# Optimization experiments

Hardware: AMD Instinct MI355X
Metric: run time of the kernel (lower is better)

Reference implementation:

```python
import jax, jax.numpy as jnp
import numpy as np

L, B, H, NI, V = 256, 32, 1024, 1024, 10000


def setup_inputs() -> dict:
    key = jax.random.key(0)
    ks = jax.random.split(key, 8)
    return {
        "input_ids": jax.random.randint(ks[0], (L, B), 0, V),
        "h0": jnp.zeros((B, H), jnp.float32),
        "c0": jnp.zeros((B, H), jnp.float32),
        "emb_w": jax.random.uniform(ks[1], (V, NI), jnp.float32, -0.1, 0.1),
        "w_ih": jax.random.normal(ks[2], (4 * H, NI), jnp.float32) * 0.02,
        "w_hh": jax.random.normal(ks[3], (4 * H, H), jnp.float32) * 0.02,
        "dec_w": jax.random.uniform(ks[4], (V, H), jnp.float32, -0.1, 0.1),
        "dec_b": jnp.zeros((V,), jnp.float32),
        "W": jax.random.normal(ks[5], (H, 1), jnp.float32) * 0.1,
        "U": jax.random.normal(ks[6], (H, 1), jnp.float32) * 0.1,
    }


def reference(input_ids, h0, c0, emb_w, w_ih, w_hh, dec_w, dec_b, W, U):
    seq_len, bsz = input_ids.shape
    nhid = h0.shape[1]
    emb = emb_w[input_ids]  # [L, B, NI]

    def lstm_cell(x, h, c):
        # torch LSTMCell (bias=False), gate order i, f, g, o
        gates = x @ w_ih.T + h @ w_hh.T  # [B, 4H]
        i, f, g, o = jnp.split(gates, 4, axis=-1)
        c_new = jax.nn.sigmoid(f) * c + jax.nn.sigmoid(i) * jnp.tanh(g)
        h_new = jax.nn.sigmoid(o) * jnp.tanh(c_new)
        return h_new, c_new

    time_idx = jnp.arange(seq_len)

    def step(carry, xs):
        h, c, hist = carry  # hist: [L, B, H] padded history of hiddens
        x, i = xs
        h, c = lstm_cell(x, h, c)
        hist = hist.at[i].set(h)
        # additive attention over all hiddens so far
        b = (hist.reshape(-1, nhid) @ U).reshape(seq_len, bsz)  # [L, B]
        a = (h @ W).reshape(1, bsz)  # [1, B]
        scores = jnp.tanh(a + b)
        scores = jnp.where((time_idx <= i)[:, None], scores, -jnp.inf)
        att = jax.nn.softmax(scores, axis=0)  # softmax over time
        ctx = jnp.sum(att[:, :, None] * hist, axis=0)  # [B, H]
        return (h, c, hist), ctx

    hist0 = jnp.zeros((seq_len, bsz, nhid), dtype=h0.dtype)
    (h, c, _), ctx = jax.lax.scan(step, (h0, c0, hist0), (emb, time_idx))
    # ctx: [L, B, H]
    logits = ctx @ dec_w.T + dec_b  # [L, B, V]
    out = jax.nn.log_softmax(logits, axis=-1)
    return out, (h, c)
```

## Files before the change

kernel.cpp:

```cpp
#include <hip/hip_runtime.h>
#include <math.h>

typedef unsigned short u16;
typedef unsigned u32;
typedef float f32x4 __attribute__((ext_vector_type(4)));
typedef float f32x2 __attribute__((ext_vector_type(2)));
typedef __bf16 bf16x8 __attribute__((ext_vector_type(8)));
typedef u16 u16x8 __attribute__((ext_vector_type(8)));
typedef u16 u16x4 __attribute__((ext_vector_type(4)));
typedef u32 u32x4 __attribute__((ext_vector_type(4)));

#define L_SEQ 256
#define BSZ 32
#define HID 1024
#define NIN 1024
#define VOC 10000
#define G4 4096
#define MROWS 8192
#define NB 64
#define DPB 16
#define SENT 0xFFFFFFFFu

__device__ __forceinline__ u16 f2bf(float f) {
    unsigned u = __float_as_uint(f);
    unsigned r = u + 0x7FFFu + ((u >> 16) & 1u);
    return (u16)(r >> 16);
}
#define BF2F(x) __builtin_bit_cast(float, (u32)((u16)(x)) << 16)

__device__ __forceinline__ float fast_sigm(float x) {
    x = fminf(fmaxf(x, -15.f), 15.f);
    return __builtin_amdgcn_rcpf(1.f + __expf(-x));
}
__device__ __forceinline__ float fast_tanh(float x) {
    x = fminf(fmaxf(x, -15.f), 15.f);
    float t = __expf(2.f * x);
    return (t - 1.f) * __builtin_amdgcn_rcpf(t + 1.f);
}
__device__ __forceinline__ unsigned umax4(u16x8 v) {
    u32x4 c = __builtin_bit_cast(u32x4, v);
    unsigned a = c.x > c.y ? c.x : c.y;
    unsigned b = c.z > c.w ? c.z : c.w;
    return a > b ? a : b;
}

__global__ __launch_bounds__(256) void cvt_bf16_kernel(const float* __restrict__ in,
                                                       u16* __restrict__ out, int n4) {
    int idx = blockIdx.x * 256 + threadIdx.x;
    if (idx < n4) {
        f32x4 v = *(const f32x4*)(in + (size_t)idx * 4);
        u16x4 o = {f2bf(v.x), f2bf(v.y), f2bf(v.z), f2bf(v.w)};
        *(u16x4*)(out + (size_t)idx * 4) = o;
    }
}

__global__ __launch_bounds__(256) void gather_emb_kernel(const int* __restrict__ ids,
                                                         const float* __restrict__ emb_w,
                                                         u16* __restrict__ out) {
    int m = blockIdx.x;
    int id = ids[m];
    const float* src = emb_w + (size_t)id * NIN;
    u16* dst = out + (size_t)m * NIN;
    int t = threadIdx.x;
    f32x4 v = *(const f32x4*)(src + t * 4);
    u16x4 o = {f2bf(v.x), f2bf(v.y), f2bf(v.z), f2bf(v.w)};
    *(u16x4*)(dst + t * 4) = o;
}

__global__ __launch_bounds__(256) void gemm_gxT_kernel(const u16* __restrict__ A,
                                                       const u16* __restrict__ B,
                                                       float* __restrict__ gxT) {
    int m0 = blockIdx.x * 128;
    int n0 = blockIdx.y * 128;
    __shared__ alignas(16) u16 As[128][40];
    __shared__ alignas(16) u16 Bs[128][40];
    int t = threadIdx.x;
    int lane = t & 63, wave = t >> 6;
    int wr = wave >> 1, wc = wave & 1;
    int l15 = lane & 15, l4 = lane >> 4;

    f32x4 acc[4][4];
    f32x4 zv = {0.f, 0.f, 0.f, 0.f};
    for (int mi = 0; mi < 4; ++mi)
        for (int ni = 0; ni < 4; ++ni) acc[mi][ni] = zv;

    for (int k0 = 0; k0 < NIN; k0 += 32) {
        for (int s = 0; s < 2; ++s) {
            int task = t + s * 256;
            int row = task >> 2, kof = (task & 3) * 8;
            *(u16x8*)(&As[row][kof]) = *(const u16x8*)(A + (size_t)(m0 + row) * NIN + k0 + kof);
            *(u16x8*)(&Bs[row][kof]) = *(const u16x8*)(B + (size_t)(n0 + row) * NIN + k0 + kof);
        }
        __syncthreads();
        bf16x8 af[4], bfr[4];
        for (int mi = 0; mi < 4; ++mi)
            af[mi] = __builtin_bit_cast(bf16x8, *(const u16x8*)(&As[wr * 64 + mi * 16 + l15][l4 * 8]));
        for (int ni = 0; ni < 4; ++ni)
            bfr[ni] = __builtin_bit_cast(bf16x8, *(const u16x8*)(&Bs[wc * 64 + ni * 16 + l15][l4 * 8]));
        for (int mi = 0; mi < 4; ++mi)
            for (int ni = 0; ni < 4; ++ni)
                acc[mi][ni] = __builtin_amdgcn_mfma_f32_16x16x32_bf16(af[mi], bfr[ni], acc[mi][ni], 0, 0, 0);
        __syncthreads();
    }
    for (int mi = 0; mi < 4; ++mi)
        for (int ni = 0; ni < 4; ++ni) {
            int n = n0 + wc * 64 + ni * 16 + l15;
            int g = n >> 10, dd = n & 1023;
            int dblk = dd >> 4, dl = dd & 15;
            int mbase = m0 + wr * 64 + mi * 16 + l4 * 4;
            int i = mbase >> 5, bb = mbase & 31;
            size_t idx = ((((size_t)dblk * L_SEQ + i) * 4 + g) * 16 + dl) * 32 + bb;
            *(f32x4*)(&gxT[idx]) = acc[mi][ni];
        }
}

__global__ __launch_bounds__(256) void gemm_bt_kernel(const u16* __restrict__ A,
                                                      const u16* __restrict__ B,
                                                      float* __restrict__ C,
                                                      const float* __restrict__ bias,
                                                      int M, int N, int K) {
    int m0 = blockIdx.x * 128;
    int n0 = blockIdx.y * 128;
    __shared__ alignas(16) u16 As[128][40];
    __shared__ alignas(16) u16 Bs[128][40];
    int t = threadIdx.x;
    int lane = t & 63, wave = t >> 6;
    int wr = wave >> 1, wc = wave & 1;
    int l15 = lane & 15, l4 = lane >> 4;

    f32x4 acc[4][4];
    f32x4 zv = {0.f, 0.f, 0.f, 0.f};
    for (int mi = 0; mi < 4; ++mi)
        for (int ni = 0; ni < 4; ++ni) acc[mi][ni] = zv;

    for (int k0 = 0; k0 < K; k0 += 32) {
        for (int s = 0; s < 2; ++s) {
            int task = t + s * 256;
            int row = task >> 2, kof = (task & 3) * 8;
            u16x8 av = *(const u16x8*)(A + (size_t)(m0 + row) * K + k0 + kof);
            *(u16x8*)(&As[row][kof]) = av;
            int brow = n0 + row;
            u16x8 bv = {0, 0, 0, 0, 0, 0, 0, 0};
            if (brow < N) bv = *(const u16x8*)(B + (size_t)brow * K + k0 + kof);
            *(u16x8*)(&Bs[row][kof]) = bv;
        }
        __syncthreads();
        bf16x8 af[4], bfr[4];
        for (int mi = 0; mi < 4; ++mi)
            af[mi] = __builtin_bit_cast(bf16x8, *(const u16x8*)(&As[wr * 64 + mi * 16 + l15][l4 * 8]));
        for (int ni = 0; ni < 4; ++ni)
            bfr[ni] = __builtin_bit_cast(bf16x8, *(const u16x8*)(&Bs[wc * 64 + ni * 16 + l15][l4 * 8]));
        for (int mi = 0; mi < 4; ++mi)
            for (int ni = 0; ni < 4; ++ni)
                acc[mi][ni] = __builtin_amdgcn_mfma_f32_16x16x32_bf16(af[mi], bfr[ni], acc[mi][ni], 0, 0, 0);
        __syncthreads();
    }

    for (int mi = 0; mi < 4; ++mi)
        for (int ni = 0; ni < 4; ++ni) {
            int col = n0 + wc * 64 + ni * 16 + l15;
            if (col < N) {
                float bb = bias ? bias[col] : 0.f;
                int rbase = m0 + wr * 64 + mi * 16 + l4 * 4;
                for (int r = 0; r < 4; ++r)
                    C[(size_t)(rbase + r) * N + col] = acc[mi][ni][r] + bb;
            }
        }
}

__global__ __launch_bounds__(256, 1) void lstm_seq_kernel(
    const float* __restrict__ c0, const u16* __restrict__ w_hh_bf,
    const float* __restrict__ gxT, const float* __restrict__ Wv, const float* __restrict__ Uv,
    u16* __restrict__ hb_hist, float* __restrict__ out_tail, float* __restrict__ part_ab) {
    __shared__ alignas(16) u16 Bs[64][1024];
    __shared__ float gsm[4][32][17];
    __shared__ float c_sl[32][17];

    int blk = blockIdx.x;
    int d0 = blk * DPB;
    int t = threadIdx.x;
    int lane = t & 63, wave = t >> 6;
    int wm = wave & 1, wn = wave >> 1;
    int l15 = lane & 15, l4 = lane >> 4;

    for (int s = 0; s < 32; ++s) {
        int cid = t + s * 256;
        int c = cid >> 7;
        int ch = cid & 127;
        int g = c >> 4, dl = c & 15;
        u16x8 v = *(const u16x8*)(w_hh_bf + (size_t)(g * HID + d0 + dl) * HID + ch * 8);
        int chs = ch ^ (c & 7);
        *(u16x8*)(&Bs[c][chs * 8]) = v;
    }
    for (int s = t; s < 512; s += 256) {
        int b = s >> 4, dl = s & 15;
        c_sl[b][dl] = c0[b * HID + d0 + dl];
    }
    __syncthreads();

    int cA = wn * 32 + l15;
    int cB = cA + 16;
    int sw = cA & 7;
    int gA = cA >> 4, dA = cA & 15;
    int gB = cB >> 4, dB = cB & 15;

    int bb = t >> 3;
    int pr = t & 7;
    int dl0 = pr * 2;

    const float* gxTb = gxT + (size_t)blk * ((size_t)L_SEQ * 2048) + wm * 16 + l4 * 4;

    f32x4 gxa0 = *(const f32x4*)(gxTb + (size_t)0 * 2048 + gA * 512 + dA * 32);
    f32x4 gxa1 = *(const f32x4*)(gxTb + (size_t)0 * 2048 + gB * 512 + dB * 32);

    for (int i = 0; i < L_SEQ; ++i) {
        const u16* hb = hb_hist + (size_t)i * (BSZ * HID);
        const u16* aptr = hb + (size_t)(wm * 16 + l15) * HID + l4 * 8;

        u16x8 afr[32];
#pragma unroll
        for (int kk = 0; kk < 32; ++kk)
            asm volatile("global_load_dwordx4 %0, %1, off offset:%c2 sc0 sc1"
                         : "=v"(afr[kk])
                         : "v"(aptr), "n"(kk * 64));

        f32x4 acc0 = {0.f, 0.f, 0.f, 0.f}, acc1 = {0.f, 0.f, 0.f, 0.f};
        unsigned pend = 0xFFFFFFFFu;
        for (;;) {
            asm volatile("s_waitcnt vmcnt(0)" ::: "memory");
            __builtin_amdgcn_sched_barrier(0);
            unsigned done = 0;
#pragma unroll
            for (int kk = 0; kk < 32; ++kk) {
                if (pend & (1u << kk)) {
                    if (__ballot(umax4(afr[kk]) == SENT) == 0) {
                        bf16x8 af = __builtin_bit_cast(bf16x8, afr[kk]);
                        int ch = kk * 4 + l4;
                        bf16x8 b0 = __builtin_bit_cast(bf16x8, *(const u16x8*)(&Bs[cA][(ch ^ sw) * 8]));
                        bf16x8 b1 = __builtin_bit_cast(bf16x8, *(const u16x8*)(&Bs[cB][(ch ^ sw) * 8]));
                        acc0 = __builtin_amdgcn_mfma_f32_16x16x32_bf16(af, b0, acc0, 0, 0, 0);
                        acc1 = __builtin_amdgcn_mfma_f32_16x16x32_bf16(af, b1, acc1, 0, 0, 0);
                        done |= 1u << kk;
                    }
                }
            }
            pend &= ~done;
            if (!pend) break;
#pragma unroll
            for (int kk = 0; kk < 32; ++kk)
                if (pend & (1u << kk))
                    asm volatile("global_load_dwordx4 %0, %1, off offset:%c2 sc0 sc1"
                                 : "=v"(afr[kk])
                                 : "v"(aptr), "n"(kk * 64));
            __builtin_amdgcn_s_sleep(1);
        }
        __builtin_amdgcn_sched_barrier(0);

#pragma unroll
        for (int r = 0; r < 4; ++r) {
            int m = wm * 16 + l4 * 4 + r;
            gsm[gA][m][dA] = acc0[r] + gxa0[r];
            gsm[gB][m][dB] = acc1[r] + gxa1[r];
        }
        __syncthreads();

        u16* hb_next = hb_hist + (size_t)(i + 1) * (BSZ * HID);
        float hn01[2];
#pragma unroll
        for (int q = 0; q < 2; ++q) {
            int dl = dl0 + q;
            float ig = gsm[0][bb][dl], fg = gsm[1][bb][dl];
            float gg = gsm[2][bb][dl], og = gsm[3][bb][dl];
            float cn = fast_sigm(fg) * c_sl[bb][dl] + fast_sigm(ig) * fast_tanh(gg);
            float hn = fast_sigm(og) * fast_tanh(cn);
            c_sl[bb][dl] = cn;
            hn01[q] = hn;
        }
        unsigned pk = (unsigned)f2bf(hn01[0]) | ((unsigned)f2bf(hn01[1]) << 16);
        __hip_atomic_store((unsigned*)(hb_next + bb * HID + d0 + dl0), pk,
                           __ATOMIC_RELAXED, __HIP_MEMORY_SCOPE_AGENT);
        if (i == L_SEQ - 1) {
            f32x2 hv = {hn01[0], hn01[1]};
            *(f32x2*)(out_tail + (size_t)bb * HID + d0 + dl0) = hv;
        }
        float pa = hn01[0] * Wv[d0 + dl0] + hn01[1] * Wv[d0 + dl0 + 1];
        float pb = hn01[0] * Uv[d0 + dl0] + hn01[1] * Uv[d0 + dl0 + 1];
        pa += __shfl_xor(pa, 1); pb += __shfl_xor(pb, 1);
        pa += __shfl_xor(pa, 2); pb += __shfl_xor(pb, 2);
        pa += __shfl_xor(pa, 4); pb += __shfl_xor(pb, 4);
        if (pr == 0) {
            f32x2 pv = {pa, pb};
            *(f32x2*)(part_ab + (((size_t)i * NB + blk) * BSZ + bb) * 2) = pv;
        }

        int inx = (i + 1 < L_SEQ) ? i + 1 : i;
        gxa0 = *(const f32x4*)(gxTb + (size_t)inx * 2048 + gA * 512 + dA * 32);
        gxa1 = *(const f32x4*)(gxTb + (size_t)inx * 2048 + gB * 512 + dB * 32);
    }

    for (int s = t; s < 512; s += 256) {
        int b2 = s >> 4, dl = s & 15;
        out_tail[(size_t)BSZ * HID + b2 * HID + d0 + dl] = c_sl[b2][dl];
    }
}

__global__ __launch_bounds__(256) void reduce_ab_kernel(const float* __restrict__ part_ab,
                                                        float* __restrict__ a_arr,
                                                        float* __restrict__ b_arr) {
    int i = blockIdx.x;
    int t = threadIdx.x;
    int b = t & 31, q = t >> 5;
    float sa = 0.f, sb = 0.f;
    for (int j = 0; j < 8; ++j) {
        int blk = q * 8 + j;
        f32x2 v = *(const f32x2*)(part_ab + (((size_t)i * NB + blk) * BSZ + b) * 2);
        sa += v.x;
        sb += v.y;
    }
    __shared__ float ra[8][32], rb[8][32];
    ra[q][b] = sa;
    rb[q][b] = sb;
    __syncthreads();
    if (q == 0) {
        for (int j = 1; j < 8; ++j) { sa += ra[j][b]; sb += rb[j][b]; }
        a_arr[i * BSZ + b] = sa;
        b_arr[i * BSZ + b] = sb;
    }
}

__global__ __launch_bounds__(256) void attn_kernel(const float* __restrict__ a_arr,
                                                   const float* __restrict__ b_arr,
                                                   const u16* __restrict__ hb_hist,
                                                   u16* __restrict__ ctx_bf) {
    int b = blockIdx.y;
    int i0 = blockIdx.x * 8;
    int t = threadIdx.x;
    __shared__ float att[8][256];
    __shared__ float red[256];

    float bt = b_arr[t * BSZ + b];
    for (int q = 0; q < 8; ++q) {
        int iq = i0 + q;
        att[q][t] = (t <= iq) ? tanhf(a_arr[iq * BSZ + b] + bt) : -INFINITY;
    }
    __syncthreads();
    for (int q = 0; q < 8; ++q) {
        int iq = i0 + q;
        red[t] = att[q][t];
        __syncthreads();
        for (int s = 128; s > 0; s >>= 1) {
            if (t < s) red[t] = fmaxf(red[t], red[t + s]);
            __syncthreads();
        }
        float m = red[0];
        __syncthreads();
        float e = (t <= iq) ? expf(att[q][t] - m) : 0.f;
        red[t] = e;
        __syncthreads();
        for (int s = 128; s > 0; s >>= 1) {
            if (t < s) red[t] += red[t + s];
            __syncthreads();
        }
        float sum = red[0];
        __syncthreads();
        att[q][t] = e / sum;
        __syncthreads();
    }

    int hc = t * 4;
    f32x4 accq[8];
    f32x4 zv = {0.f, 0.f, 0.f, 0.f};
    for (int q = 0; q < 8; ++q) accq[q] = zv;
    int imax = i0 + 7;
    for (int t2 = 0; t2 <= imax; ++t2) {
        u16x4 hq = *(const u16x4*)(hb_hist + (size_t)(t2 + 1) * (BSZ * HID) + (size_t)b * HID + hc);
        f32x4 hv = {BF2F(hq.x), BF2F(hq.y), BF2F(hq.z), BF2F(hq.w)};
        for (int q = 0; q < 8; ++q) accq[q] += hv * att[q][t2];
    }
    for (int q = 0; q < 8; ++q) {
        size_t row = (size_t)(i0 + q) * BSZ + b;
        u16x4 o = {f2bf(accq[q].x), f2bf(accq[q].y), f2bf(accq[q].z), f2bf(accq[q].w)};
        *(u16x4*)(ctx_bf + row * HID + hc) = o;
    }
}

__global__ __launch_bounds__(256) void logsoftmax_kernel(float* __restrict__ x, int V) {
    int row = blockIdx.x;
    float* p = x + (size_t)row * V;
    __shared__ float red[256];
    int t = threadIdx.x;
    float frag[40];
    float m = -INFINITY;
#pragma unroll
    for (int k = 0; k < 40; ++k) {
        int j = t + k * 256;
        if (j < VOC) {
            frag[k] = p[j];
            m = fmaxf(m, frag[k]);
        }
    }
    red[t] = m;
    __syncthreads();
    for (int s = 128; s > 0; s >>= 1) {
        if (t < s) red[t] = fmaxf(red[t], red[t + s]);
        __syncthreads();
    }
    m = red[0];
    __syncthreads();
    float sum = 0.f;
#pragma unroll
    for (int k = 0; k < 40; ++k) {
        int j = t + k * 256;
        if (j < VOC) sum += __expf(frag[k] - m);
    }
    red[t] = sum;
    __syncthreads();
    for (int s = 128; s > 0; s >>= 1) {
        if (t < s) red[t] += red[t + s];
        __syncthreads();
    }
    float lse = m + logf(red[0]);
#pragma unroll
    for (int k = 0; k < 40; ++k) {
        int j = t + k * 256;
        if (j < VOC) p[j] = frag[k] - lse;
    }
}

extern "C" void kernel_launch(void* const* d_in, const int* in_sizes, int n_in,
                              void* d_out, int out_size, void* d_ws, size_t ws_size,
                              hipStream_t stream) {
    const int* ids = (const int*)d_in[0];
    const float* h0 = (const float*)d_in[1];
    const float* c0 = (const float*)d_in[2];
    const float* emb_w = (const float*)d_in[3];
    const float* w_ih = (const float*)d_in[4];
    const float* w_hh = (const float*)d_in[5];
    const float* dec_w = (const float*)d_in[6];
    const float* dec_b = (const float*)d_in[7];
    const float* Wv = (const float*)d_in[8];
    const float* Uv = (const float*)d_in[9];

    char* p = (char*)d_ws;
    auto alloc = [&](size_t bytes) {
        void* r = (void*)p;
        p += (bytes + 255) & ~(size_t)255;
        return r;
    };
    u16* w_ih_bf = (u16*)alloc((size_t)G4 * NIN * 2);
    u16* w_hh_bf = (u16*)alloc((size_t)G4 * HID * 2);
    u16* dec_w_bf = (u16*)alloc((size_t)VOC * HID * 2);
    char* hbreg = (char*)alloc((size_t)(L_SEQ + 1) * BSZ * HID * 2);
    u16* ctx_bf = (u16*)alloc((size_t)MROWS * HID * 2);
    float* part_ab = (float*)alloc((size_t)L_SEQ * NB * BSZ * 2 * 4);
    float* a_arr = (float*)alloc((size_t)L_SEQ * BSZ * 4);
    float* b_arr = (float*)alloc((size_t)L_SEQ * BSZ * 4);

    u16* A_emb = (u16*)hbreg;
    u16* hb_hist = (u16*)hbreg;
    float* out = (float*)d_out;
    float* gxT = out;
    float* out_tail = out + (size_t)MROWS * VOC;

    cvt_bf16_kernel<<<G4 * NIN / 1024, 256, 0, stream>>>(w_ih, w_ih_bf, G4 * NIN / 4);
    cvt_bf16_kernel<<<G4 * HID / 1024, 256, 0, stream>>>(w_hh, w_hh_bf, G4 * HID / 4);
    cvt_bf16_kernel<<<(VOC * HID / 4 + 255) / 256, 256, 0, stream>>>(dec_w, dec_w_bf, VOC * HID / 4);
    gather_emb_kernel<<<MROWS, 256, 0, stream>>>(ids, emb_w, A_emb);
    gemm_gxT_kernel<<<dim3(MROWS / 128, G4 / 128), 256, 0, stream>>>(A_emb, w_ih_bf, gxT);

    hipMemsetAsync(hb_hist + (size_t)BSZ * HID, 0xFF, (size_t)L_SEQ * BSZ * HID * 2, stream);
    cvt_bf16_kernel<<<BSZ * HID / 1024, 256, 0, stream>>>(h0, hb_hist, BSZ * HID / 4);

    {
        const float* c0a = c0;
        const u16* whha = w_hh_bf;
        const float* gxa = gxT;
        const float* Wa = Wv;
        const float* Ua = Uv;
        u16* hba = hb_hist;
        float* tail = out_tail;
        float* pab = part_ab;
        void* args[] = {&c0a, &whha, &gxa, &Wa, &Ua, &hba, &tail, &pab};
        hipLaunchCooperativeKernel((const void*)lstm_seq_kernel, dim3(NB), dim3(256), args, 0,
                                   stream);
    }
    reduce_ab_kernel<<<L_SEQ, 256, 0, stream>>>(part_ab, a_arr, b_arr);
    attn_kernel<<<dim3(L_SEQ / 8, BSZ), 256, 0, stream>>>(a_arr, b_arr, hb_hist, ctx_bf);
    gemm_bt_kernel<<<dim3(MROWS / 128, (VOC + 127) / 128), 256, 0, stream>>>(ctx_bf, dec_w_bf, out,
                                                                             dec_b, MROWS, VOC, HID);
    logsoftmax_kernel<<<MROWS, 256, 0, stream>>>(out, VOC);
}
```

Before: 2.605 ms.

## Overlap input-projection GEMM with LSTM recurrence via producer blocks and sentinel polling

Removes the separate input-projection GEMM launch and runs it inside the recurrent kernel on 160 extra worker blocks, which write the gate pre-activations as bf16 with atomic stores. The 64 recurrent blocks poll a sentinel-filled buffer before consuming each timestep's values, so the GEMM can overlap the serial recurrence. The projection output is also stored in bf16 instead of fp32, halving its traffic, at some cost in precision. The kernel is now a normal launch rather than a cooperative one, so correctness depends on the producer blocks being co-resident with the recurrent blocks and making progress; otherwise it could deadlock.

```diff
diff --git a/kernel.cpp b/kernel.cpp
--- a/kernel.cpp
+++ b/kernel.cpp
@@ -3,12 +3,14 @@
 
 typedef unsigned short u16;
 typedef unsigned u32;
+typedef unsigned long long u64;
 typedef float f32x4 __attribute__((ext_vector_type(4)));
 typedef float f32x2 __attribute__((ext_vector_type(2)));
 typedef __bf16 bf16x8 __attribute__((ext_vector_type(8)));
 typedef u16 u16x8 __attribute__((ext_vector_type(8)));
 typedef u16 u16x4 __attribute__((ext_vector_type(4)));
 typedef u32 u32x4 __attribute__((ext_vector_type(4)));
+typedef u32 u32x2 __attribute__((ext_vector_type(2)));
 
 #define L_SEQ 256
 #define BSZ 32
@@ -18,6 +20,7 @@
 #define G4 4096
 #define MROWS 8192
 #define NB 64
+#define NW 160
 #define DPB 16
 #define SENT 0xFFFFFFFFu
 
@@ -65,53 +68,6 @@
     f32x4 v = *(const f32x4*)(src + t * 4);
     u16x4 o = {f2bf(v.x), f2bf(v.y), f2bf(v.z), f2bf(v.w)};
     *(u16x4*)(dst + t * 4) = o;
-}
-
-__global__ __launch_bounds__(256) void gemm_gxT_kernel(const u16* __restrict__ A,
-                                                       const u16* __restrict__ B,
-                                                       float* __restrict__ gxT) {
-    int m0 = blockIdx.x * 128;
-    int n0 = blockIdx.y * 128;
-    __shared__ alignas(16) u16 As[128][40];
-    __shared__ alignas(16) u16 Bs[128][40];
-    int t = threadIdx.x;
-    int lane = t & 63, wave = t >> 6;
-    int wr = wave >> 1, wc = wave & 1;
-    int l15 = lane & 15, l4 = lane >> 4;
-
-    f32x4 acc[4][4];
-    f32x4 zv = {0.f, 0.f, 0.f, 0.f};
-    for (int mi = 0; mi < 4; ++mi)
-        for (int ni = 0; ni < 4; ++ni) acc[mi][ni] = zv;
-
-    for (int k0 = 0; k0 < NIN; k0 += 32) {
-        for (int s = 0; s < 2; ++s) {
-            int task = t + s * 256;
-            int row = task >> 2, kof = (task & 3) * 8;
-            *(u16x8*)(&As[row][kof]) = *(const u16x8*)(A + (size_t)(m0 + row) * NIN + k0 + kof);
-            *(u16x8*)(&Bs[row][kof]) = *(const u16x8*)(B + (size_t)(n0 + row) * NIN + k0 + kof);
-        }
-        __syncthreads();
-        bf16x8 af[4], bfr[4];
-        for (int mi = 0; mi < 4; ++mi)
-            af[mi] = __builtin_bit_cast(bf16x8, *(const u16x8*)(&As[wr * 64 + mi * 16 + l15][l4 * 8]));
-        for (int ni = 0; ni < 4; ++ni)
-            bfr[ni] = __builtin_bit_cast(bf16x8, *(const u16x8*)(&Bs[wc * 64 + ni * 16 + l15][l4 * 8]));
-        for (int mi = 0; mi < 4; ++mi)
-            for (int ni = 0; ni < 4; ++ni)
-                acc[mi][ni] = __builtin_amdgcn_mfma_f32_16x16x32_bf16(af[mi], bfr[ni], acc[mi][ni], 0, 0, 0);
-        __syncthreads();
-    }
-    for (int mi = 0; mi < 4; ++mi)
-        for (int ni = 0; ni < 4; ++ni) {
-            int n = n0 + wc * 64 + ni * 16 + l15;
-            int g = n >> 10, dd = n & 1023;
-            int dblk = dd >> 4, dl = dd & 15;
-            int mbase = m0 + wr * 64 + mi * 16 + l4 * 4;
-            int i = mbase >> 5, bb = mbase & 31;
-            size_t idx = ((((size_t)dblk * L_SEQ + i) * 4 + g) * 16 + dl) * 32 + bb;
-            *(f32x4*)(&gxT[idx]) = acc[mi][ni];
-        }
 }
 
 __global__ __launch_bounds__(256) void gemm_bt_kernel(const u16* __restrict__ A,
@@ -169,19 +125,73 @@
 }
 
 __global__ __launch_bounds__(256, 1) void lstm_seq_kernel(
-    const float* __restrict__ c0, const u16* __restrict__ w_hh_bf,
-    const float* __restrict__ gxT, const float* __restrict__ Wv, const float* __restrict__ Uv,
-    u16* __restrict__ hb_hist, float* __restrict__ out_tail, float* __restrict__ part_ab) {
+    const float* __restrict__ c0, const u16* __restrict__ w_hh_bf, u16* __restrict__ gxT,
+    const float* __restrict__ Wv, const float* __restrict__ Uv, u16* __restrict__ hb_hist,
+    float* __restrict__ out_tail, float* __restrict__ part_ab, const u16* __restrict__ A_emb,
+    const u16* __restrict__ w_ih_bf) {
     __shared__ alignas(16) u16 Bs[64][1024];
     __shared__ float gsm[4][32][17];
     __shared__ float c_sl[32][17];
 
     int blk = blockIdx.x;
-    int d0 = blk * DPB;
     int t = threadIdx.x;
     int lane = t & 63, wave = t >> 6;
+    int l15 = lane & 15, l4 = lane >> 4;
+
+    if (blk >= NB) {
+        u16(*As2)[40] = (u16(*)[40])(&Bs[0][0]);
+        u16(*Bs2)[40] = (u16(*)[40])((char*)(&Bs[0][0]) + 10240);
+        int wr = wave >> 1, wc = wave & 1;
+        for (int tau = blk - NB; tau < 2048; tau += NW) {
+            int m0 = (tau >> 5) * 128;
+            int n0 = (tau & 31) * 128;
+            f32x4 acc[4][4];
+            f32x4 zv = {0.f, 0.f, 0.f, 0.f};
+            for (int mi = 0; mi < 4; ++mi)
+                for (int ni = 0; ni < 4; ++ni) acc[mi][ni] = zv;
+            for (int k0 = 0; k0 < NIN; k0 += 32) {
+                for (int s = 0; s < 2; ++s) {
+                    int task = t + s * 256;
+                    int row = task >> 2, kof = (task & 3) * 8;
+                    *(u16x8*)(&As2[row][kof]) =
+                        *(const u16x8*)(A_emb + (size_t)(m0 + row) * NIN + k0 + kof);
+                    *(u16x8*)(&Bs2[row][kof]) =
+                        *(const u16x8*)(w_ih_bf + (size_t)(n0 + row) * NIN + k0 + kof);
+                }
+                __syncthreads();
+                bf16x8 af[4], bfr[4];
+                for (int mi = 0; mi < 4; ++mi)
+                    af[mi] = __builtin_bit_cast(bf16x8,
+                                                *(const u16x8*)(&As2[wr * 64 + mi * 16 + l15][l4 * 8]));
+                for (int ni = 0; ni < 4; ++ni)
+                    bfr[ni] = __builtin_bit_cast(bf16x8,
+                                                 *(const u16x8*)(&Bs2[wc * 64 + ni * 16 + l15][l4 * 8]));
+                for (int mi = 0; mi < 4; ++mi)
+                    for (int ni = 0; ni < 4; ++ni)
+                        acc[mi][ni] =
+                            __builtin_amdgcn_mfma_f32_16x16x32_bf16(af[mi], bfr[ni], acc[mi][ni], 0, 0, 0);
+                __syncthreads();
+            }
+            for (int mi = 0; mi < 4; ++mi)
+                for (int ni = 0; ni < 4; ++ni) {
+                    int n = n0 + wc * 64 + ni * 16 + l15;
+                    int g = n >> 10, dd = n & 1023;
+                    int dblk = dd >> 4, dl = dd & 15;
+                    int mbase = m0 + wr * 64 + mi * 16 + l4 * 4;
+                    int i = mbase >> 5, bb2 = mbase & 31;
+                    size_t idx = ((((size_t)dblk * L_SEQ + i) * 4 + g) * 16 + dl) * 32 + bb2;
+                    u32 lo = (u32)f2bf(acc[mi][ni][0]) | ((u32)f2bf(acc[mi][ni][1]) << 16);
+                    u32 hi = (u32)f2bf(acc[mi][ni][2]) | ((u32)f2bf(acc[mi][ni][3]) << 16);
+                    u64 pk = (u64)lo | ((u64)hi << 32);
+                    __hip_atomic_store((u64*)(gxT + idx), pk, __ATOMIC_RELAXED,
+                                       __HIP_MEMORY_SCOPE_AGENT);
+                }
+        }
+        return;
+    }
+
+    int d0 = blk * DPB;
     int wm = wave & 1, wn = wave >> 1;
-    int l15 = lane & 15, l4 = lane >> 4;
 
     for (int s = 0; s < 32; ++s) {
         int cid = t + s * 256;
@@ -208,14 +218,21 @@
     int pr = t & 7;
     int dl0 = pr * 2;
 
-    const float* gxTb = gxT + (size_t)blk * ((size_t)L_SEQ * 2048) + wm * 16 + l4 * 4;
-
-    f32x4 gxa0 = *(const f32x4*)(gxTb + (size_t)0 * 2048 + gA * 512 + dA * 32);
-    f32x4 gxa1 = *(const f32x4*)(gxTb + (size_t)0 * 2048 + gB * 512 + dB * 32);
+    const u16* gxTb = gxT + (size_t)blk * ((size_t)L_SEQ * 2048) + wm * 16 + l4 * 4;
+
+    u16x4 gw0, gw1;
+    {
+        const u16* p0 = gxTb + gA * 512 + dA * 32;
+        const u16* p1 = gxTb + gB * 512 + dB * 32;
+        asm volatile("global_load_dwordx2 %0, %1, off sc0 sc1" : "=v"(gw0) : "v"(p0));
+        asm volatile("global_load_dwordx2 %0, %1, off sc0 sc1" : "=v"(gw1) : "v"(p1));
+    }
 
     for (int i = 0; i < L_SEQ; ++i) {
         const u16* hb = hb_hist + (size_t)i * (BSZ * HID);
         const u16* aptr = hb + (size_t)(wm * 16 + l15) * HID + l4 * 8;
+        const u16* cp0 = gxTb + (size_t)i * 2048 + gA * 512 + dA * 32;
+        const u16* cp1 = gxTb + (size_t)i * 2048 + gB * 512 + dB * 32;
 
         u16x8 afr[32];
 #pragma unroll
@@ -256,11 +273,22 @@
         }
         __builtin_amdgcn_sched_barrier(0);
 
+        for (;;) {
+            u32x2 w0 = __builtin_bit_cast(u32x2, gw0);
+            u32x2 w1 = __builtin_bit_cast(u32x2, gw1);
+            if (__ballot(w0.x == SENT || w0.y == SENT || w1.x == SENT || w1.y == SENT) == 0) break;
+            __builtin_amdgcn_s_sleep(4);
+            asm volatile("global_load_dwordx2 %0, %1, off sc0 sc1" : "=v"(gw0) : "v"(cp0));
+            asm volatile("global_load_dwordx2 %0, %1, off sc0 sc1" : "=v"(gw1) : "v"(cp1));
+            asm volatile("s_waitcnt vmcnt(0)" ::: "memory");
+            __builtin_amdgcn_sched_barrier(0);
+        }
+
 #pragma unroll
         for (int r = 0; r < 4; ++r) {
             int m = wm * 16 + l4 * 4 + r;
-            gsm[gA][m][dA] = acc0[r] + gxa0[r];
-            gsm[gB][m][dB] = acc1[r] + gxa1[r];
+            gsm[gA][m][dA] = acc0[r] + BF2F(gw0[r]);
+            gsm[gB][m][dB] = acc1[r] + BF2F(gw1[r]);
         }
         __syncthreads();
 
@@ -293,9 +321,13 @@
             *(f32x2*)(part_ab + (((size_t)i * NB + blk) * BSZ + bb) * 2) = pv;
         }
 
-        int inx = (i + 1 < L_SEQ) ? i + 1 : i;
-        gxa0 = *(const f32x4*)(gxTb + (size_t)inx * 2048 + gA * 512 + dA * 32);
-        gxa1 = *(const f32x4*)(gxTb + (size_t)inx * 2048 + gB * 512 + dB * 32);
+        {
+            int inx = (i + 1 < L_SEQ) ? i + 1 : i;
+            const u16* np0 = gxTb + (size_t)inx * 2048 + gA * 512 + dA * 32;
+            const u16* np1 = gxTb + (size_t)inx * 2048 + gB * 512 + dB * 32;
+            asm volatile("global_load_dwordx2 %0, %1, off sc0 sc1" : "=v"(gw0) : "v"(np0));
+            asm volatile("global_load_dwordx2 %0, %1, off sc0 sc1" : "=v"(gw1) : "v"(np1));
+        }
     }
 
     for (int s = t; s < 512; s += 256) {
@@ -450,40 +482,29 @@
     u16* w_ih_bf = (u16*)alloc((size_t)G4 * NIN * 2);
     u16* w_hh_bf = (u16*)alloc((size_t)G4 * HID * 2);
     u16* dec_w_bf = (u16*)alloc((size_t)VOC * HID * 2);
-    char* hbreg = (char*)alloc((size_t)(L_SEQ + 1) * BSZ * HID * 2);
+    u16* hb_hist = (u16*)alloc((size_t)(L_SEQ + 1) * BSZ * HID * 2);
+    u16* A_emb = (u16*)alloc((size_t)MROWS * NIN * 2);
     u16* ctx_bf = (u16*)alloc((size_t)MROWS * HID * 2);
     float* part_ab = (float*)alloc((size_t)L_SEQ * NB * BSZ * 2 * 4);
     float* a_arr = (float*)alloc((size_t)L_SEQ * BSZ * 4);
     float* b_arr = (float*)alloc((size_t)L_SEQ * BSZ * 4);
 
-    u16* A_emb = (u16*)hbreg;
-    u16* hb_hist = (u16*)hbreg;
     float* out = (float*)d_out;
-    float* gxT = out;
+    u16* gxT = (u16*)d_out;
     float* out_tail = out + (size_t)MROWS * VOC;
 
     cvt_bf16_kernel<<<G4 * NIN / 1024, 256, 0, stream>>>(w_ih, w_ih_bf, G4 * NIN / 4);
     cvt_bf16_kernel<<<G4 * HID / 1024, 256, 0, stream>>>(w_hh, w_hh_bf, G4 * HID / 4);
     cvt_bf16_kernel<<<(VOC * HID / 4 + 255) / 256, 256, 0, stream>>>(dec_w, dec_w_bf, VOC * HID / 4);
     gather_emb_kernel<<<MROWS, 256, 0, stream>>>(ids, emb_w, A_emb);
-    gemm_gxT_kernel<<<dim3(MROWS / 128, G4 / 128), 256, 0, stream>>>(A_emb, w_ih_bf, gxT);
-
+
+    hipMemsetAsync(gxT, 0xFF, (size_t)MROWS * G4 * 2, stream);
     hipMemsetAsync(hb_hist + (size_t)BSZ * HID, 0xFF, (size_t)L_SEQ * BSZ * HID * 2, stream);
     cvt_bf16_kernel<<<BSZ * HID / 1024, 256, 0, stream>>>(h0, hb_hist, BSZ * HID / 4);
 
-    {
-        const float* c0a = c0;
-        const u16* whha = w_hh_bf;
-        const float* gxa = gxT;
-        const float* Wa = Wv;
-        const float* Ua = Uv;
-        u16* hba = hb_hist;
-        float* tail = out_tail;
-        float* pab = part_ab;
-        void* args[] = {&c0a, &whha, &gxa, &Wa, &Ua, &hba, &tail, &pab};
-        hipLaunchCooperativeKernel((const void*)lstm_seq_kernel, dim3(NB), dim3(256), args, 0,
-                                   stream);
-    }
+    lstm_seq_kernel<<<dim3(NB + NW), dim3(256), 0, stream>>>(c0, w_hh_bf, gxT, Wv, Uv, hb_hist,
+                                                             out_tail, part_ab, A_emb, w_ih_bf);
+
     reduce_ab_kernel<<<L_SEQ, 256, 0, stream>>>(part_ab, a_arr, b_arr);
     attn_kernel<<<dim3(L_SEQ / 8, BSZ), 256, 0, stream>>>(a_arr, b_arr, hb_hist, ctx_bf);
     gemm_bt_kernel<<<dim3(MROWS / 128, (VOC + 127) / 128), 256, 0, stream>>>(ctx_bf, dec_w_bf, out,
```

After: 2.517 ms. 3.4% less time.
